# Optimization experiments

Measured on AMD Instinct MI355X. Metric: run time of the kernel, lower is better.

Reference implementation:

```python
import jax, jax.numpy as jnp
import numpy as np

E = 16           # num_experts
D = 4096         # hidden_size
F = 688          # per-expert SwiGLU intermediate size
N = 8192         # total tokens (bsz*seq_len)
CAP_FACTOR = 1.25


def setup_inputs() -> dict:
    key = jax.random.key(0)
    k1, k2, k3, k4, k5, k6 = jax.random.split(key, 6)
    return {
        "x": jax.random.normal(k1, (N, D), dtype=jnp.float32),
        "topk_idx": jax.random.randint(k2, (N,), 0, E, dtype=jnp.int32),
        "topk_scores": jax.random.uniform(k3, (N,), dtype=jnp.float32),
        "Wg": jax.random.normal(k4, (E, D, F), dtype=jnp.float32) * 0.02,
        "Wu": jax.random.normal(k5, (E, D, F), dtype=jnp.float32) * 0.02,
        "Wd": jax.random.normal(k6, (E, F, D), dtype=jnp.float32) * 0.02,
    }


def reference(x, topk_idx, topk_scores, Wg, Wu, Wd):
    # Switch-style top-1 MoE with capacity-based token dropping.
    # Deterministic variant: tokens beyond capacity are dropped in token order
    # (original uses randperm; the math pattern is identical).
    n, d = x.shape
    e = Wg.shape[0]
    cap = int(CAP_FACTOR * n / e)  # static under jit

    # position of each token within its assigned expert (0-based)
    oh = jax.nn.one_hot(topk_idx, e, dtype=jnp.int32)            # [N, E]
    pos = jnp.take_along_axis(jnp.cumsum(oh, axis=0) - 1,
                              topk_idx[:, None].astype(jnp.int32), axis=1)[:, 0]
    keep = pos < cap                                             # [N] bool

    # dispatch: scatter kept tokens into [E, cap, D]; dropped go to dummy row E
    e_safe = jnp.where(keep, topk_idx, e)
    p_safe = jnp.minimum(pos, cap - 1)
    buf = jnp.zeros((e + 1, cap, d), x.dtype).at[e_safe, p_safe].set(x)[:e]

    # per-expert SwiGLU FFN: down(silu(gate(x)) * up(x))
    h = jax.nn.silu(jnp.einsum('ecd,edf->ecf', buf, Wg)) \
        * jnp.einsum('ecd,edf->ecf', buf, Wu)                    # [E, cap, F]
    out = jnp.einsum('ecf,efd->ecd', h, Wd)                      # [E, cap, D]

    # combine: gather back, zero-pad dropped tokens, scale by gate scores
    y = out[topk_idx, p_safe] * keep[:, None].astype(x.dtype)
    y = y * topk_scores[:, None]
    return y
```

## Files before the change

kernel.cpp:

```cpp
#include <hip/hip_runtime.h>
#include <hip/hip_bf16.h>

#define E_ 16
#define D_ 4096
#define F_ 688
#define N_ 8192
#define CAP_ 640
#define NKT_ 64
#define NFT_ 11

typedef __attribute__((ext_vector_type(8))) short bf16x8;
typedef __attribute__((ext_vector_type(4))) float f32x4;
typedef __attribute__((ext_vector_type(4))) float fvec4;
typedef __attribute__((ext_vector_type(8))) unsigned short usvec8;

__device__ __forceinline__ unsigned short f2bf(float f) {
    __hip_bfloat16 h = __float2bfloat16(f);
    return __builtin_bit_cast(unsigned short, h);
}
__device__ __forceinline__ int lidx(int row, int k) {
    return row * 64 + (((k >> 3) ^ (row & 7)) << 3) + (k & 7);
}
__device__ __forceinline__ int bidx(int row, int k) {
    return row * 64 + (((k >> 3) ^ ((row >> 1) & 7)) << 3) + (k & 7);
}
__device__ __forceinline__ void gload16(const unsigned short* g, unsigned short* l) {
    __builtin_amdgcn_global_load_lds(
        (const __attribute__((address_space(1))) unsigned int*)g,
        (__attribute__((address_space(3))) unsigned int*)l, 16, 0, 0);
}

#define WAITV(N) asm volatile("s_waitcnt vmcnt(" #N ")" ::: "memory")
#define SBAR     __builtin_amdgcn_s_barrier()
#define SCHED0   __builtin_amdgcn_sched_barrier(0)

__global__ void k_dispatch(const int* __restrict__ idx,
                           int* __restrict__ slot_token,
                           int* __restrict__ row_of,
                           int* __restrict__ cnt) {
    __shared__ int hist[256][E_];
    const int t = threadIdx.x;
#pragma unroll
    for (int e = 0; e < E_; e++) hist[t][e] = 0;
    __syncthreads();
    const int base = t * (N_ / 256);
    for (int j = 0; j < N_ / 256; j++) {
        int e = idx[base + j];
        hist[t][e]++;
    }
    __syncthreads();
    if (t < E_) {
        int run = 0;
        for (int i = 0; i < 256; i++) { int v = hist[i][t]; hist[i][t] = run; run += v; }
        cnt[t] = run < CAP_ ? run : CAP_;
    }
    for (int s = t; s < E_ * CAP_; s += 256) slot_token[s] = -1;
    __syncthreads();
    for (int j = 0; j < N_ / 256; j++) {
        int i = base + j;
        int e = idx[i];
        int p = hist[t][e]++;
        if (p < CAP_) { slot_token[e * CAP_ + p] = i; row_of[i] = e * CAP_ + p; }
        else          { row_of[i] = -1; }
    }
}

__global__ void k_zero_dropped(const int* __restrict__ row_of, float* __restrict__ y) {
    const int i = blockIdx.x;
    if (row_of[i] >= 0) return;
    fvec4* yp = (fvec4*)(y + (size_t)i * D_);
    fvec4 z = {0.f, 0.f, 0.f, 0.f};
    for (int c = threadIdx.x; c < D_ / 4; c += 256) yp[c] = z;
}

__global__ void k_gather(const float* __restrict__ x, const int* __restrict__ slot_token,
                         unsigned short* __restrict__ Aimg) {
    const int strip = blockIdx.y;
    const int kg = blockIdx.x;
    const int t = threadIdx.x;
    const int r = t >> 1, h = t & 1;
    const int tok = slot_token[strip * 128 + r];
#pragma unroll
    for (int kl4 = 0; kl4 < 4; kl4++) {
        const int kt = kg * 4 + kl4;
        const int k0 = kt * 64 + h * 32;
        unsigned short* dst = Aimg + ((size_t)strip * NKT_ + kt) * 8192;
        usvec8 p[4];
        if (tok < 0) {
            usvec8 z = {0, 0, 0, 0, 0, 0, 0, 0};
            p[0] = z; p[1] = z; p[2] = z; p[3] = z;
        } else {
            const float* src = x + (size_t)tok * D_ + k0;
#pragma unroll
            for (int uu = 0; uu < 4; uu++) {
                fvec4 a = *(const fvec4*)(src + uu * 8);
                fvec4 b = *(const fvec4*)(src + uu * 8 + 4);
                usvec8 q = {f2bf(a[0]), f2bf(a[1]), f2bf(a[2]), f2bf(a[3]),
                            f2bf(b[0]), f2bf(b[1]), f2bf(b[2]), f2bf(b[3])};
                p[uu] = q;
            }
        }
#pragma unroll
        for (int uu = 0; uu < 4; uu++)
            *(usvec8*)&dst[lidx(r, h * 32 + uu * 8)] = p[uu];
    }
}

__global__ void k_wprep_gu(const float* __restrict__ Wg, const float* __restrict__ Wu,
                           unsigned short* __restrict__ img) {
    const int ft = blockIdx.x, kt = blockIdx.y, e = blockIdx.z;
    const int tid = threadIdx.x;
    const int fpos = (tid & 31) * 2, kq8 = (tid >> 5) * 8;
    const int gf = ft * 64 + fpos;
    const bool v = gf < F_;
    const float2 fz2 = {0.f, 0.f};
    float2 g[8], u[8];
#pragma unroll
    for (int r = 0; r < 8; r++) {
        size_t off = (size_t)e * D_ * F_ + (size_t)(kt * 64 + kq8 + r) * F_ + gf;
        g[r] = v ? *(const float2*)(Wg + off) : fz2;
        u[r] = v ? *(const float2*)(Wu + off) : fz2;
    }
    usvec8 pg0, pg1, pu0, pu1;
#pragma unroll
    for (int r = 0; r < 8; r++) {
        pg0[r] = (short)f2bf(g[r].x); pg1[r] = (short)f2bf(g[r].y);
        pu0[r] = (short)f2bf(u[r].x); pu1[r] = (short)f2bf(u[r].y);
    }
    unsigned short* t = img + ((size_t)(e * NKT_ + kt) * NFT_ + ft) * 8192;
    *(usvec8*)&t[bidx(fpos, kq8)]            = pg0;
    *(usvec8*)&t[bidx(fpos + 1, kq8)]        = pg1;
    *(usvec8*)&t[4096 + bidx(fpos, kq8)]     = pu0;
    *(usvec8*)&t[4096 + bidx(fpos + 1, kq8)] = pu1;
}

__global__ void k_wprep_d(const float* __restrict__ Wd, unsigned short* __restrict__ img) {
    const int dt = blockIdx.x, kt = blockIdx.y, e = blockIdx.z;
    const int tid = threadIdx.x;
    const int dpos = (tid & 31) * 2, kq8 = (tid >> 5) * 8;
    const int gd = dt * 64 + dpos;
    const float2 fz2 = {0.f, 0.f};
    float2 b[8];
#pragma unroll
    for (int r = 0; r < 8; r++) {
        int krow = kt * 64 + kq8 + r;
        b[r] = (krow < F_) ? *(const float2*)(Wd + (size_t)e * F_ * D_ + (size_t)krow * D_ + gd) : fz2;
    }
    usvec8 p0, p1;
#pragma unroll
    for (int r = 0; r < 8; r++) { p0[r] = (short)f2bf(b[r].x); p1[r] = (short)f2bf(b[r].y); }
    unsigned short* t = img + ((size_t)(e * NFT_ + kt) * 64 + dt) * 4096;
    *(usvec8*)&t[bidx(dpos, kq8)]     = p0;
    *(usvec8*)&t[bidx(dpos + 1, kq8)] = p1;
}

__global__ __launch_bounds__(256, 2) void k_gemm1_dma(
    const unsigned short* __restrict__ Aimg, const unsigned short* __restrict__ Wgu,
    const int* __restrict__ cnt, unsigned short* __restrict__ Himg) {
    const int bid = blockIdx.x;
    const int xcd = bid & 7;
    const int j = bid >> 3;
    const int mb = j % 5;
    const int gl = j / 5;
    const int group = xcd * 22 + gl;
    const int e = group / NFT_, fidx = group % NFT_;
    const int m0 = mb * 128;
    if (m0 >= cnt[e]) return;
    const int strip = e * 5 + mb;

    __shared__ __align__(16) unsigned short As[2][8192];
    __shared__ __align__(16) unsigned short Bgs[3][4096];
    __shared__ __align__(16) unsigned short Bus[3][4096];

    const int tid = threadIdx.x;
    const int lane = tid & 63, wave = tid >> 6;
    const int wm = wave >> 1, wn = wave & 1;
    const int aw4 = wave * 4, bw2 = wave * 2;

    f32x4 accG[4][2], accU[4][2];
#pragma unroll
    for (int a = 0; a < 4; a++)
#pragma unroll
        for (int b = 0; b < 2; b++) {
            f32x4 z = {0.f, 0.f, 0.f, 0.f};
            accG[a][b] = z; accU[a][b] = z;
        }

    const unsigned short* Astrip = Aimg + (size_t)strip * NKT_ * 8192;
    const unsigned short* WguE = Wgu + (size_t)e * NKT_ * NFT_ * 8192 + (size_t)fidx * 8192;

#define G1_A(T, BUF)                                                           \
    {                                                                          \
        const unsigned short* asrc = Astrip + (size_t)(T) * 8192;              \
        _Pragma("unroll") for (int i = 0; i < 4; i++)                          \
            gload16(asrc + (aw4 + i) * 512 + lane * 8, &As[BUF][(aw4 + i) * 512]); \
    }
#define G1_B(T, BUF)                                                           \
    {                                                                          \
        const unsigned short* bsrc = WguE + (size_t)(T) * (NFT_ * 8192);       \
        _Pragma("unroll") for (int i = 0; i < 2; i++)                          \
            gload16(bsrc + (bw2 + i) * 512 + lane * 8, &Bgs[BUF][(bw2 + i) * 512]); \
        _Pragma("unroll") for (int i = 0; i < 2; i++)                          \
            gload16(bsrc + 4096 + (bw2 + i) * 512 + lane * 8, &Bus[BUF][(bw2 + i) * 512]); \
    }

    G1_A(0, 0)
    G1_B(0, 0)
    G1_B(1, 1)
    WAITV(4);
    SBAR;

    for (int kt = 0; kt < NKT_; ++kt) {
        const int curA = kt & 1, curB = kt % 3;
        if (kt + 1 < NKT_) G1_A(kt + 1, (kt + 1) & 1)
        if (kt + 2 < NKT_) G1_B(kt + 2, (kt + 2) % 3)
        SCHED0;
        __builtin_amdgcn_s_setprio(1);
#pragma unroll
        for (int kk = 0; kk < 64; kk += 32) {
            const int ko = kk + ((lane >> 4) << 3);
            bf16x8 av[4], bgv[2], buv[2];
#pragma unroll
            for (int mi = 0; mi < 4; mi++)
                av[mi] = *(const bf16x8*)&As[curA][lidx(wm * 64 + mi * 16 + (lane & 15), ko)];
#pragma unroll
            for (int ni = 0; ni < 2; ni++) {
                int rr = wn * 32 + ni * 16 + (lane & 15);
                bgv[ni] = *(const bf16x8*)&Bgs[curB][bidx(rr, ko)];
                buv[ni] = *(const bf16x8*)&Bus[curB][bidx(rr, ko)];
            }
#pragma unroll
            for (int mi = 0; mi < 4; mi++)
#pragma unroll
                for (int ni = 0; ni < 2; ni++) {
                    accG[mi][ni] = __builtin_amdgcn_mfma_f32_16x16x32_bf16(av[mi], bgv[ni], accG[mi][ni], 0, 0, 0);
                    accU[mi][ni] = __builtin_amdgcn_mfma_f32_16x16x32_bf16(av[mi], buv[ni], accU[mi][ni], 0, 0, 0);
                }
        }
        __builtin_amdgcn_s_setprio(0);
        SCHED0;
        if (kt + 2 < NKT_) WAITV(4); else WAITV(0);
        if (kt + 1 < NKT_) SBAR;
    }
#undef G1_A
#undef G1_B

    unsigned short* Ht = Himg + ((size_t)strip * NFT_ + fidx) * 8192;
#pragma unroll
    for (int mi = 0; mi < 4; mi++)
#pragma unroll
        for (int ni = 0; ni < 2; ni++) {
            int fl = wn * 32 + ni * 16 + (lane & 15);
            int rl = wm * 64 + mi * 16 + ((lane >> 4) << 2);
#pragma unroll
            for (int q = 0; q < 4; q++) {
                float g = accG[mi][ni][q], u = accU[mi][ni][q];
                float h = g * u / (1.f + __expf(-g));
                Ht[lidx(rl + q, fl)] = f2bf(h);
            }
        }
}

__global__ __launch_bounds__(256, 2) void k_gemm2_dma(
    const unsigned short* __restrict__ Himg, const unsigned short* __restrict__ WdI,
    const int* __restrict__ slot_token, const int* __restrict__ cnt,
    const float* __restrict__ scores, float* __restrict__ y) {
    const int bid = blockIdx.x;
    const int xcd = bid & 7;
    const int j = bid >> 3;
    const int mb = j % 5;
    const int gl = j / 5;
    const int group = xcd * 128 + gl;
    const int e = group >> 6, didx = group & 63;
    const int m0 = mb * 128, d0 = didx * 64;
    if (m0 >= cnt[e]) return;
    const int strip = e * 5 + mb;

    __shared__ __align__(16) unsigned short As[2][8192];
    __shared__ __align__(16) unsigned short Bts[3][4096];
    __shared__ int tokS[128];
    __shared__ float scS[128];

    const int tid = threadIdx.x;
    const int lane = tid & 63, wave = tid >> 6;
    const int wm = wave >> 1, wn = wave & 1;
    const int aw4 = wave * 4, bw2 = wave * 2;

    if (tid < 128) {
        int t = slot_token[e * CAP_ + m0 + tid];
        tokS[tid] = t;
        scS[tid] = (t >= 0) ? scores[t] : 0.f;
    }
    __syncthreads();

    f32x4 acc[4][2];
#pragma unroll
    for (int a = 0; a < 4; a++)
#pragma unroll
        for (int b = 0; b < 2; b++) {
            f32x4 z = {0.f, 0.f, 0.f, 0.f};
            acc[a][b] = z;
        }

    const unsigned short* Hstrip = Himg + (size_t)strip * NFT_ * 8192;
    const unsigned short* WdE = WdI + (size_t)e * NFT_ * 64 * 4096 + (size_t)didx * 4096;

#define G2_A(T, BUF)                                                           \
    {                                                                          \
        const unsigned short* asrc = Hstrip + (size_t)(T) * 8192;              \
        _Pragma("unroll") for (int i = 0; i < 4; i++)                          \
            gload16(asrc + (aw4 + i) * 512 + lane * 8, &As[BUF][(aw4 + i) * 512]); \
    }
#define G2_B(T, BUF)                                                           \
    {                                                                          \
        const unsigned short* bsrc = WdE + (size_t)(T) * (64 * 4096);          \
        _Pragma("unroll") for (int i = 0; i < 2; i++)                          \
            gload16(bsrc + (bw2 + i) * 512 + lane * 8, &Bts[BUF][(bw2 + i) * 512]); \
    }

    G2_A(0, 0)
    G2_B(0, 0)
    G2_B(1, 1)
    WAITV(2);
    SBAR;

    for (int fc = 0; fc < NFT_; ++fc) {
        const int curA = fc & 1, curB = fc % 3;
        if (fc + 1 < NFT_) G2_A(fc + 1, (fc + 1) & 1)
        if (fc + 2 < NFT_) G2_B(fc + 2, (fc + 2) % 3)
        SCHED0;
        __builtin_amdgcn_s_setprio(1);
#pragma unroll
        for (int kk = 0; kk < 64; kk += 32) {
            const int ko = kk + ((lane >> 4) << 3);
            bf16x8 av[4], bv[2];
#pragma unroll
            for (int mi = 0; mi < 4; mi++)
                av[mi] = *(const bf16x8*)&As[curA][lidx(wm * 64 + mi * 16 + (lane & 15), ko)];
#pragma unroll
            for (int ni = 0; ni < 2; ni++)
                bv[ni] = *(const bf16x8*)&Bts[curB][bidx(wn * 32 + ni * 16 + (lane & 15), ko)];
#pragma unroll
            for (int mi = 0; mi < 4; mi++)
#pragma unroll
                for (int ni = 0; ni < 2; ni++)
                    acc[mi][ni] = __builtin_amdgcn_mfma_f32_16x16x32_bf16(av[mi], bv[ni], acc[mi][ni], 0, 0, 0);
        }
        __builtin_amdgcn_s_setprio(0);
        SCHED0;
        if (fc + 2 < NFT_) WAITV(2); else WAITV(0);
        if (fc + 1 < NFT_) SBAR;
    }
#undef G2_A
#undef G2_B

#pragma unroll
    for (int mi = 0; mi < 4; mi++)
#pragma unroll
        for (int ni = 0; ni < 2; ni++) {
            int d = d0 + wn * 32 + ni * 16 + (lane & 15);
            int rowb = wm * 64 + mi * 16 + ((lane >> 4) << 2);
#pragma unroll
            for (int q = 0; q < 4; q++) {
                int row = rowb + q;
                int t = tokS[row];
                if (t >= 0) y[(size_t)t * D_ + d] = acc[mi][ni][q] * scS[row];
            }
        }
}

extern "C" void kernel_launch(void* const* d_in, const int* in_sizes, int n_in,
                              void* d_out, int out_size, void* d_ws, size_t ws_size,
                              hipStream_t stream) {
    const float* x   = (const float*)d_in[0];
    const int*   idx = (const int*)d_in[1];
    const float* sc  = (const float*)d_in[2];
    const float* Wg  = (const float*)d_in[3];
    const float* Wu  = (const float*)d_in[4];
    const float* Wd  = (const float*)d_in[5];
    float* y = (float*)d_out;

    char* ws = (char*)d_ws;
    int* slot_token = (int*)ws;
    int* row_of     = (int*)(ws + 40960);
    int* cnt        = (int*)(ws + 40960 + 32768);
    const size_t hoff   = 131072;
    const size_t hbytes = (size_t)80 * NFT_ * 16384;
    unsigned short* Himg = (unsigned short*)(ws + hoff);
    const size_t aoff   = hoff + hbytes;
    const size_t abytes = (size_t)80 * NKT_ * 16384;
    unsigned short* Aimg = (unsigned short*)(ws + aoff);
    const size_t guoff   = aoff + abytes;
    const size_t gubytes = (size_t)E_ * NKT_ * NFT_ * 16384;
    unsigned short* WguI = (unsigned short*)(ws + guoff);
    const size_t wdoff   = guoff + gubytes;
    unsigned short* WdI  = (unsigned short*)(ws + wdoff);

    k_dispatch<<<1, 256, 0, stream>>>(idx, slot_token, row_of, cnt);
    k_zero_dropped<<<N_, 256, 0, stream>>>(row_of, y);
    k_gather<<<dim3(16, 80), 256, 0, stream>>>(x, slot_token, Aimg);
    k_wprep_gu<<<dim3(NFT_, NKT_, E_), 256, 0, stream>>>(Wg, Wu, WguI);
    k_wprep_d<<<dim3(64, NFT_, E_), 256, 0, stream>>>(Wd, WdI);
    k_gemm1_dma<<<880, 256, 0, stream>>>(Aimg, WguI, cnt, Himg);
    k_gemm2_dma<<<5120, 256, 0, stream>>>(Himg, WdI, slot_token, cnt, sc, y);
}
```

Measured before the change: 554.1 us.

## Switch to K=32 MFMA-native tile layout with triple buffering and higher occupancy

Repacks the activation, weight and intermediate images into 32-wide K tiles laid out so each MFMA fragment is a contiguous 8-element load, which removes the XOR swizzle index math. Both GEMMs now use a single 3-stage buffer ring with half-size tiles, which lowers LDS use and lets launch bounds rise to 3 and 4 blocks per CU. The weight-prep kernels switch to float4 loads. The zero-dropped kernel becomes grid-strided over 128 blocks. The risks are more loop iterations and barriers per K extent, and possible LDS bank conflicts without the swizzle.

```diff
diff --git a/kernel.cpp b/kernel.cpp
--- a/kernel.cpp
+++ b/kernel.cpp
@@ -6,23 +6,19 @@
 #define F_ 688
 #define N_ 8192
 #define CAP_ 640
-#define NKT_ 64
 #define NFT_ 11
+#define NKT32_ 128
+#define NFT32_ 22
 
 typedef __attribute__((ext_vector_type(8))) short bf16x8;
 typedef __attribute__((ext_vector_type(4))) float f32x4;
 typedef __attribute__((ext_vector_type(4))) float fvec4;
+typedef __attribute__((ext_vector_type(4))) unsigned short usvec4;
 typedef __attribute__((ext_vector_type(8))) unsigned short usvec8;
 
 __device__ __forceinline__ unsigned short f2bf(float f) {
     __hip_bfloat16 h = __float2bfloat16(f);
     return __builtin_bit_cast(unsigned short, h);
-}
-__device__ __forceinline__ int lidx(int row, int k) {
-    return row * 64 + (((k >> 3) ^ (row & 7)) << 3) + (k & 7);
-}
-__device__ __forceinline__ int bidx(int row, int k) {
-    return row * 64 + (((k >> 3) ^ ((row >> 1) & 7)) << 3) + (k & 7);
 }
 __device__ __forceinline__ void gload16(const unsigned short* g, unsigned short* l) {
     __builtin_amdgcn_global_load_lds(
@@ -33,6 +29,7 @@
 #define WAITV(N) asm volatile("s_waitcnt vmcnt(" #N ")" ::: "memory")
 #define SBAR     __builtin_amdgcn_s_barrier()
 #define SCHED0   __builtin_amdgcn_sched_barrier(0)
+
 
 __global__ void k_dispatch(const int* __restrict__ idx,
                            int* __restrict__ slot_token,
@@ -66,11 +63,12 @@
 }
 
 __global__ void k_zero_dropped(const int* __restrict__ row_of, float* __restrict__ y) {
-    const int i = blockIdx.x;
-    if (row_of[i] >= 0) return;
-    fvec4* yp = (fvec4*)(y + (size_t)i * D_);
-    fvec4 z = {0.f, 0.f, 0.f, 0.f};
-    for (int c = threadIdx.x; c < D_ / 4; c += 256) yp[c] = z;
+    for (int i = blockIdx.x; i < N_; i += gridDim.x) {
+        if (row_of[i] >= 0) continue;
+        fvec4* yp = (fvec4*)(y + (size_t)i * D_);
+        fvec4 z = {0.f, 0.f, 0.f, 0.f};
+        for (int c = threadIdx.x; c < D_ / 4; c += 256) yp[c] = z;
+    }
 }
 
 __global__ void k_gather(const float* __restrict__ x, const int* __restrict__ slot_token,
@@ -81,28 +79,27 @@
     const int r = t >> 1, h = t & 1;
     const int tok = slot_token[strip * 128 + r];
 #pragma unroll
-    for (int kl4 = 0; kl4 < 4; kl4++) {
-        const int kt = kg * 4 + kl4;
-        const int k0 = kt * 64 + h * 32;
-        unsigned short* dst = Aimg + ((size_t)strip * NKT_ + kt) * 8192;
-        usvec8 p[4];
+    for (int i = 0; i < 8; i++) {
+        const int kt = kg * 8 + i;
+        unsigned short* dst = Aimg + ((size_t)strip * NKT32_ + kt) * 4096;
+        usvec8 p0, p1;
         if (tok < 0) {
             usvec8 z = {0, 0, 0, 0, 0, 0, 0, 0};
-            p[0] = z; p[1] = z; p[2] = z; p[3] = z;
+            p0 = z; p1 = z;
         } else {
-            const float* src = x + (size_t)tok * D_ + k0;
-#pragma unroll
-            for (int uu = 0; uu < 4; uu++) {
-                fvec4 a = *(const fvec4*)(src + uu * 8);
-                fvec4 b = *(const fvec4*)(src + uu * 8 + 4);
-                usvec8 q = {f2bf(a[0]), f2bf(a[1]), f2bf(a[2]), f2bf(a[3]),
-                            f2bf(b[0]), f2bf(b[1]), f2bf(b[2]), f2bf(b[3])};
-                p[uu] = q;
-            }
-        }
-#pragma unroll
-        for (int uu = 0; uu < 4; uu++)
-            *(usvec8*)&dst[lidx(r, h * 32 + uu * 8)] = p[uu];
+            const float* src = x + (size_t)tok * D_ + kt * 32 + h * 16;
+            fvec4 a = *(const fvec4*)(src);
+            fvec4 b = *(const fvec4*)(src + 4);
+            fvec4 c = *(const fvec4*)(src + 8);
+            fvec4 d = *(const fvec4*)(src + 12);
+            usvec8 q0 = {f2bf(a[0]), f2bf(a[1]), f2bf(a[2]), f2bf(a[3]),
+                         f2bf(b[0]), f2bf(b[1]), f2bf(b[2]), f2bf(b[3])};
+            usvec8 q1 = {f2bf(c[0]), f2bf(c[1]), f2bf(c[2]), f2bf(c[3]),
+                         f2bf(d[0]), f2bf(d[1]), f2bf(d[2]), f2bf(d[3])};
+            p0 = q0; p1 = q1;
+        }
+        *(usvec8*)&dst[(2 * h) * 1024 + r * 8]     = p0;
+        *(usvec8*)&dst[(2 * h + 1) * 1024 + r * 8] = p1;
     }
 }
 
@@ -110,51 +107,52 @@
                            unsigned short* __restrict__ img) {
     const int ft = blockIdx.x, kt = blockIdx.y, e = blockIdx.z;
     const int tid = threadIdx.x;
-    const int fpos = (tid & 31) * 2, kq8 = (tid >> 5) * 8;
-    const int gf = ft * 64 + fpos;
+    const int f4 = (tid & 15) * 4, kq4 = (tid >> 4) * 4;
+    const int gf = ft * 64 + f4;
     const bool v = gf < F_;
-    const float2 fz2 = {0.f, 0.f};
-    float2 g[8], u[8];
-#pragma unroll
-    for (int r = 0; r < 8; r++) {
-        size_t off = (size_t)e * D_ * F_ + (size_t)(kt * 64 + kq8 + r) * F_ + gf;
-        g[r] = v ? *(const float2*)(Wg + off) : fz2;
-        u[r] = v ? *(const float2*)(Wu + off) : fz2;
-    }
-    usvec8 pg0, pg1, pu0, pu1;
-#pragma unroll
-    for (int r = 0; r < 8; r++) {
-        pg0[r] = (short)f2bf(g[r].x); pg1[r] = (short)f2bf(g[r].y);
-        pu0[r] = (short)f2bf(u[r].x); pu1[r] = (short)f2bf(u[r].y);
-    }
-    unsigned short* t = img + ((size_t)(e * NKT_ + kt) * NFT_ + ft) * 8192;
-    *(usvec8*)&t[bidx(fpos, kq8)]            = pg0;
-    *(usvec8*)&t[bidx(fpos + 1, kq8)]        = pg1;
-    *(usvec8*)&t[4096 + bidx(fpos, kq8)]     = pu0;
-    *(usvec8*)&t[4096 + bidx(fpos + 1, kq8)] = pu1;
+    const fvec4 fz = {0.f, 0.f, 0.f, 0.f};
+    fvec4 g[4], u[4];
+#pragma unroll
+    for (int r = 0; r < 4; r++) {
+        size_t off = (size_t)e * D_ * F_ + (size_t)(kt * 64 + kq4 + r) * F_ + gf;
+        g[r] = v ? *(const fvec4*)(Wg + off) : fz;
+        u[r] = v ? *(const fvec4*)(Wu + off) : fz;
+    }
+    const int t32 = kq4 >> 5, kl = kq4 & 31;
+    unsigned short* dst = img + ((size_t)(e * NKT32_ + kt * 2 + t32) * NFT_ + ft) * 4096;
+    const int ubase = (kl >> 3) * 512 + (kl & 7);
+#pragma unroll
+    for (int i = 0; i < 4; i++) {
+        usvec4 pg = {f2bf(g[0][i]), f2bf(g[1][i]), f2bf(g[2][i]), f2bf(g[3][i])};
+        usvec4 pu = {f2bf(u[0][i]), f2bf(u[1][i]), f2bf(u[2][i]), f2bf(u[3][i])};
+        *(usvec4*)&dst[ubase + (f4 + i) * 8]        = pg;
+        *(usvec4*)&dst[2048 + ubase + (f4 + i) * 8] = pu;
+    }
 }
 
 __global__ void k_wprep_d(const float* __restrict__ Wd, unsigned short* __restrict__ img) {
     const int dt = blockIdx.x, kt = blockIdx.y, e = blockIdx.z;
     const int tid = threadIdx.x;
-    const int dpos = (tid & 31) * 2, kq8 = (tid >> 5) * 8;
-    const int gd = dt * 64 + dpos;
-    const float2 fz2 = {0.f, 0.f};
-    float2 b[8];
-#pragma unroll
-    for (int r = 0; r < 8; r++) {
-        int krow = kt * 64 + kq8 + r;
-        b[r] = (krow < F_) ? *(const float2*)(Wd + (size_t)e * F_ * D_ + (size_t)krow * D_ + gd) : fz2;
-    }
-    usvec8 p0, p1;
-#pragma unroll
-    for (int r = 0; r < 8; r++) { p0[r] = (short)f2bf(b[r].x); p1[r] = (short)f2bf(b[r].y); }
-    unsigned short* t = img + ((size_t)(e * NFT_ + kt) * 64 + dt) * 4096;
-    *(usvec8*)&t[bidx(dpos, kq8)]     = p0;
-    *(usvec8*)&t[bidx(dpos + 1, kq8)] = p1;
-}
-
-__global__ __launch_bounds__(256, 2) void k_gemm1_dma(
+    const int d4 = (tid & 15) * 4, kq4 = (tid >> 4) * 4;
+    const int gd = dt * 64 + d4;
+    const fvec4 fz = {0.f, 0.f, 0.f, 0.f};
+    fvec4 b[4];
+#pragma unroll
+    for (int r = 0; r < 4; r++) {
+        int krow = kt * 64 + kq4 + r;
+        b[r] = (krow < F_) ? *(const fvec4*)(Wd + (size_t)e * F_ * D_ + (size_t)krow * D_ + gd) : fz;
+    }
+    const int t32 = kq4 >> 5, kl = kq4 & 31;
+    unsigned short* dst = img + ((size_t)(e * NFT32_ + kt * 2 + t32) * 64 + dt) * 2048;
+    const int ubase = (kl >> 3) * 512 + (kl & 7);
+#pragma unroll
+    for (int i = 0; i < 4; i++) {
+        usvec4 p = {f2bf(b[0][i]), f2bf(b[1][i]), f2bf(b[2][i]), f2bf(b[3][i])};
+        *(usvec4*)&dst[ubase + (d4 + i) * 8] = p;
+    }
+}
+
+__global__ __launch_bounds__(256, 3) void k_gemm1_dma(
     const unsigned short* __restrict__ Aimg, const unsigned short* __restrict__ Wgu,
     const int* __restrict__ cnt, unsigned short* __restrict__ Himg) {
     const int bid = blockIdx.x;
@@ -168,14 +166,13 @@
     if (m0 >= cnt[e]) return;
     const int strip = e * 5 + mb;
 
-    __shared__ __align__(16) unsigned short As[2][8192];
-    __shared__ __align__(16) unsigned short Bgs[3][4096];
-    __shared__ __align__(16) unsigned short Bus[3][4096];
+    __shared__ __align__(16) unsigned short As[3][4096];
+    __shared__ __align__(16) unsigned short Bgu[3][4096];
 
     const int tid = threadIdx.x;
     const int lane = tid & 63, wave = tid >> 6;
     const int wm = wave >> 1, wn = wave & 1;
-    const int aw4 = wave * 4, bw2 = wave * 2;
+    const int wq = wave * 1024;
 
     f32x4 accG[4][2], accU[4][2];
 #pragma unroll
@@ -186,48 +183,42 @@
             accG[a][b] = z; accU[a][b] = z;
         }
 
-    const unsigned short* Astrip = Aimg + (size_t)strip * NKT_ * 8192;
-    const unsigned short* WguE = Wgu + (size_t)e * NKT_ * NFT_ * 8192 + (size_t)fidx * 8192;
-
-#define G1_A(T, BUF)                                                           \
+    const unsigned short* Astrip = Aimg + (size_t)strip * NKT32_ * 4096;
+    const unsigned short* WguE = Wgu + ((size_t)e * NKT32_ * NFT_ + fidx) * 4096;
+
+#define G1STAGE(T, BUF)                                                        \
     {                                                                          \
-        const unsigned short* asrc = Astrip + (size_t)(T) * 8192;              \
-        _Pragma("unroll") for (int i = 0; i < 4; i++)                          \
-            gload16(asrc + (aw4 + i) * 512 + lane * 8, &As[BUF][(aw4 + i) * 512]); \
-    }
-#define G1_B(T, BUF)                                                           \
-    {                                                                          \
-        const unsigned short* bsrc = WguE + (size_t)(T) * (NFT_ * 8192);       \
-        _Pragma("unroll") for (int i = 0; i < 2; i++)                          \
-            gload16(bsrc + (bw2 + i) * 512 + lane * 8, &Bgs[BUF][(bw2 + i) * 512]); \
-        _Pragma("unroll") for (int i = 0; i < 2; i++)                          \
-            gload16(bsrc + 4096 + (bw2 + i) * 512 + lane * 8, &Bus[BUF][(bw2 + i) * 512]); \
-    }
-
-    G1_A(0, 0)
-    G1_B(0, 0)
-    G1_B(1, 1)
+        const unsigned short* asrc = Astrip + (size_t)(T) * 4096 + wq;         \
+        gload16(asrc + lane * 8,       &As[BUF][wq]);                          \
+        gload16(asrc + 512 + lane * 8, &As[BUF][wq + 512]);                    \
+        const unsigned short* bsrc = WguE + (size_t)(T) * (NFT_ * 4096) + wq;  \
+        gload16(bsrc + lane * 8,       &Bgu[BUF][wq]);                         \
+        gload16(bsrc + 512 + lane * 8, &Bgu[BUF][wq + 512]);                   \
+    }
+
+    G1STAGE(0, 0)
+    G1STAGE(1, 1)
     WAITV(4);
     SBAR;
 
-    for (int kt = 0; kt < NKT_; ++kt) {
-        const int curA = kt & 1, curB = kt % 3;
-        if (kt + 1 < NKT_) G1_A(kt + 1, (kt + 1) & 1)
-        if (kt + 2 < NKT_) G1_B(kt + 2, (kt + 2) % 3)
+    const int arow8 = (wm * 64 + (lane & 15)) * 8;
+    const int brow8 = (wn * 32 + (lane & 15)) * 8;
+    const int kg = lane >> 4;
+
+    for (int kt = 0; kt < NKT32_; ++kt) {
+        const int cur = kt % 3;
+        if (kt + 2 < NKT32_) G1STAGE(kt + 2, (kt + 2) % 3)
         SCHED0;
         __builtin_amdgcn_s_setprio(1);
-#pragma unroll
-        for (int kk = 0; kk < 64; kk += 32) {
-            const int ko = kk + ((lane >> 4) << 3);
+        {
             bf16x8 av[4], bgv[2], buv[2];
 #pragma unroll
             for (int mi = 0; mi < 4; mi++)
-                av[mi] = *(const bf16x8*)&As[curA][lidx(wm * 64 + mi * 16 + (lane & 15), ko)];
+                av[mi] = *(const bf16x8*)&As[cur][kg * 1024 + arow8 + mi * 128];
 #pragma unroll
             for (int ni = 0; ni < 2; ni++) {
-                int rr = wn * 32 + ni * 16 + (lane & 15);
-                bgv[ni] = *(const bf16x8*)&Bgs[curB][bidx(rr, ko)];
-                buv[ni] = *(const bf16x8*)&Bus[curB][bidx(rr, ko)];
+                bgv[ni] = *(const bf16x8*)&Bgu[cur][kg * 512 + brow8 + ni * 128];
+                buv[ni] = *(const bf16x8*)&Bgu[cur][2048 + kg * 512 + brow8 + ni * 128];
             }
 #pragma unroll
             for (int mi = 0; mi < 4; mi++)
@@ -239,29 +230,29 @@
         }
         __builtin_amdgcn_s_setprio(0);
         SCHED0;
-        if (kt + 2 < NKT_) WAITV(4); else WAITV(0);
-        if (kt + 1 < NKT_) SBAR;
-    }
-#undef G1_A
-#undef G1_B
-
-    unsigned short* Ht = Himg + ((size_t)strip * NFT_ + fidx) * 8192;
+        if (kt + 2 < NKT32_) WAITV(4); else WAITV(0);
+        if (kt + 1 < NKT32_) SBAR;
+    }
+#undef G1STAGE
+
+    unsigned short* Hs = Himg + (size_t)(strip * NFT32_ + fidx * 2) * 4096;
 #pragma unroll
     for (int mi = 0; mi < 4; mi++)
 #pragma unroll
         for (int ni = 0; ni < 2; ni++) {
             int fl = wn * 32 + ni * 16 + (lane & 15);
             int rl = wm * 64 + mi * 16 + ((lane >> 4) << 2);
+            unsigned short* Ht = Hs + (size_t)(fl >> 5) * 4096 + ((fl & 31) >> 3) * 1024 + (fl & 7);
 #pragma unroll
             for (int q = 0; q < 4; q++) {
                 float g = accG[mi][ni][q], u = accU[mi][ni][q];
                 float h = g * u / (1.f + __expf(-g));
-                Ht[lidx(rl + q, fl)] = f2bf(h);
+                Ht[(rl + q) * 8] = f2bf(h);
             }
         }
 }
 
-__global__ __launch_bounds__(256, 2) void k_gemm2_dma(
+__global__ __launch_bounds__(256, 4) void k_gemm2_dma(
     const unsigned short* __restrict__ Himg, const unsigned short* __restrict__ WdI,
     const int* __restrict__ slot_token, const int* __restrict__ cnt,
     const float* __restrict__ scores, float* __restrict__ y) {
@@ -276,15 +267,15 @@
     if (m0 >= cnt[e]) return;
     const int strip = e * 5 + mb;
 
-    __shared__ __align__(16) unsigned short As[2][8192];
-    __shared__ __align__(16) unsigned short Bts[3][4096];
+    __shared__ __align__(16) unsigned short As[3][4096];
+    __shared__ __align__(16) unsigned short Bd[3][2048];
     __shared__ int tokS[128];
     __shared__ float scS[128];
 
     const int tid = threadIdx.x;
     const int lane = tid & 63, wave = tid >> 6;
     const int wm = wave >> 1, wn = wave & 1;
-    const int aw4 = wave * 4, bw2 = wave * 2;
+    const int wq = wave * 1024;
 
     if (tid < 128) {
         int t = slot_token[e * CAP_ + m0 + tid];
@@ -302,44 +293,40 @@
             acc[a][b] = z;
         }
 
-    const unsigned short* Hstrip = Himg + (size_t)strip * NFT_ * 8192;
-    const unsigned short* WdE = WdI + (size_t)e * NFT_ * 64 * 4096 + (size_t)didx * 4096;
-
-#define G2_A(T, BUF)                                                           \
+    const unsigned short* Hstrip = Himg + (size_t)strip * NFT32_ * 4096;
+    const unsigned short* WdE = WdI + ((size_t)e * NFT32_ * 64 + didx) * 2048;
+
+#define G2STAGE(T, BUF)                                                        \
     {                                                                          \
-        const unsigned short* asrc = Hstrip + (size_t)(T) * 8192;              \
-        _Pragma("unroll") for (int i = 0; i < 4; i++)                          \
-            gload16(asrc + (aw4 + i) * 512 + lane * 8, &As[BUF][(aw4 + i) * 512]); \
-    }
-#define G2_B(T, BUF)                                                           \
-    {                                                                          \
-        const unsigned short* bsrc = WdE + (size_t)(T) * (64 * 4096);          \
-        _Pragma("unroll") for (int i = 0; i < 2; i++)                          \
-            gload16(bsrc + (bw2 + i) * 512 + lane * 8, &Bts[BUF][(bw2 + i) * 512]); \
-    }
-
-    G2_A(0, 0)
-    G2_B(0, 0)
-    G2_B(1, 1)
-    WAITV(2);
+        const unsigned short* asrc = Hstrip + (size_t)(T) * 4096 + wq;         \
+        gload16(asrc + lane * 8,       &As[BUF][wq]);                          \
+        gload16(asrc + 512 + lane * 8, &As[BUF][wq + 512]);                    \
+        const unsigned short* bsrc = WdE + (size_t)(T) * (64 * 2048) + wave * 512; \
+        gload16(bsrc + lane * 8, &Bd[BUF][wave * 512]);                        \
+    }
+
+    G2STAGE(0, 0)
+    G2STAGE(1, 1)
+    WAITV(3);
     SBAR;
 
-    for (int fc = 0; fc < NFT_; ++fc) {
-        const int curA = fc & 1, curB = fc % 3;
-        if (fc + 1 < NFT_) G2_A(fc + 1, (fc + 1) & 1)
-        if (fc + 2 < NFT_) G2_B(fc + 2, (fc + 2) % 3)
+    const int arow8 = (wm * 64 + (lane & 15)) * 8;
+    const int brow8 = (wn * 32 + (lane & 15)) * 8;
+    const int kg = lane >> 4;
+
+    for (int fc = 0; fc < NFT32_; ++fc) {
+        const int cur = fc % 3;
+        if (fc + 2 < NFT32_) G2STAGE(fc + 2, (fc + 2) % 3)
         SCHED0;
         __builtin_amdgcn_s_setprio(1);
-#pragma unroll
-        for (int kk = 0; kk < 64; kk += 32) {
-            const int ko = kk + ((lane >> 4) << 3);
+        {
             bf16x8 av[4], bv[2];
 #pragma unroll
             for (int mi = 0; mi < 4; mi++)
-                av[mi] = *(const bf16x8*)&As[curA][lidx(wm * 64 + mi * 16 + (lane & 15), ko)];
+                av[mi] = *(const bf16x8*)&As[cur][kg * 1024 + arow8 + mi * 128];
 #pragma unroll
             for (int ni = 0; ni < 2; ni++)
-                bv[ni] = *(const bf16x8*)&Bts[curB][bidx(wn * 32 + ni * 16 + (lane & 15), ko)];
+                bv[ni] = *(const bf16x8*)&Bd[cur][kg * 512 + brow8 + ni * 128];
 #pragma unroll
             for (int mi = 0; mi < 4; mi++)
 #pragma unroll
@@ -348,11 +335,10 @@
         }
         __builtin_amdgcn_s_setprio(0);
         SCHED0;
-        if (fc + 2 < NFT_) WAITV(2); else WAITV(0);
-        if (fc + 1 < NFT_) SBAR;
-    }
-#undef G2_A
-#undef G2_B
+        if (fc + 2 < NFT32_) WAITV(3); else WAITV(0);
+        if (fc + 1 < NFT32_) SBAR;
+    }
+#undef G2STAGE
 
 #pragma unroll
     for (int mi = 0; mi < 4; mi++)
@@ -385,21 +371,21 @@
     int* row_of     = (int*)(ws + 40960);
     int* cnt        = (int*)(ws + 40960 + 32768);
     const size_t hoff   = 131072;
-    const size_t hbytes = (size_t)80 * NFT_ * 16384;
+    const size_t hbytes = (size_t)80 * NFT32_ * 8192;
     unsigned short* Himg = (unsigned short*)(ws + hoff);
     const size_t aoff   = hoff + hbytes;
-    const size_t abytes = (size_t)80 * NKT_ * 16384;
+    const size_t abytes = (size_t)80 * NKT32_ * 8192;
     unsigned short* Aimg = (unsigned short*)(ws + aoff);
     const size_t guoff   = aoff + abytes;
-    const size_t gubytes = (size_t)E_ * NKT_ * NFT_ * 16384;
+    const size_t gubytes = (size_t)E_ * NKT32_ * NFT_ * 8192;
     unsigned short* WguI = (unsigned short*)(ws + guoff);
     const size_t wdoff   = guoff + gubytes;
     unsigned short* WdI  = (unsigned short*)(ws + wdoff);
 
     k_dispatch<<<1, 256, 0, stream>>>(idx, slot_token, row_of, cnt);
-    k_zero_dropped<<<N_, 256, 0, stream>>>(row_of, y);
+    k_zero_dropped<<<128, 256, 0, stream>>>(row_of, y);
     k_gather<<<dim3(16, 80), 256, 0, stream>>>(x, slot_token, Aimg);
-    k_wprep_gu<<<dim3(NFT_, NKT_, E_), 256, 0, stream>>>(Wg, Wu, WguI);
+    k_wprep_gu<<<dim3(NFT_, 64, E_), 256, 0, stream>>>(Wg, Wu, WguI);
     k_wprep_d<<<dim3(64, NFT_, E_), 256, 0, stream>>>(Wd, WdI);
     k_gemm1_dma<<<880, 256, 0, stream>>>(Aimg, WguI, cnt, Himg);
     k_gemm2_dma<<<5120, 256, 0, stream>>>(Himg, WdI, slot_token, cnt, sc, y);
```

Measured after the change: 591.2 us. +6.7%, slower.
